# Kernel tuning notes

Measured on AMD Instinct MI355X. Metric: run time of the kernel, lower is better.

Reference implementation:

```python
import jax, jax.numpy as jnp
import numpy as np

WARMUP = 365
# param ranges (lo, hi) standing in for MODEL_PARAM_DICT['tank']['param_range'],
# order: KC W1 W2 K1 K2 a0 b0 c0 h1 h2 a1 a2 h3 b1 h4 c1 d1 e1 e2 h
_RANGES = np.array([
    [0.5, 1.5], [1.0, 100.0], [1.0, 100.0], [0.01, 1.0], [0.01, 1.0],
    [0.01, 1.0], [0.01, 1.0], [0.01, 1.0], [0.0, 90.0], [0.0, 100.0],
    [0.01, 1.0], [0.01, 1.0], [0.0, 100.0], [0.01, 1.0], [0.0, 100.0],
    [0.01, 1.0], [0.001, 1.0], [0.01, 1.0], [0.01, 1.0], [0.0, 100.0],
], dtype=np.float32)


def _tank_sim(p_and_e, parameters):
    lo = jnp.asarray(_RANGES[:, 0])
    hi = jnp.asarray(_RANGES[:, 1])
    ph = lo + parameters * (hi - lo)            # [B, 20] physical params
    (kc, w1, w2, k1, k2, a0, b0, c0p, h1, h2, a1, a2, h3, b1, h4, c1p,
     d1, e1, e2, h) = [ph[:, i] for i in range(20)]

    u = 1.0 / 1000.0        # hydrodt / 1000
    dt = 0.5 * u

    def step(carry, pe_t):
        xf, xp, x2, xs, x3, x4, x5, qs = carry
        p, e = pe_t
        # --- runoff generation (water balance) ---
        ep = kc * e
        et = jnp.minimum(ep, p + xp + xf)
        pe = jnp.clip(p - et, 0.0)
        x = xf
        xf = jnp.clip(x - jnp.clip(ep - p, 0.0), 0.0)
        xp = jnp.clip(xp - jnp.clip(ep - p - x, 0.0), 0.0)
        t1 = jnp.clip(k1 * jnp.minimum(x2, w1 - xp), 0.0)
        xp = xp + t1
        x2 = jnp.clip(x2 - t1, 0.0)
        t2 = jnp.clip(k2 * (xs * w1 - xp * w2) / (w1 + w2), 0.0)
        xp = xp + t2
        xs = jnp.clip(xs - t2, 0.0)
        xf = xf + jnp.clip(xp + pe - w1, 0.0)
        xp = jnp.minimum(w1, xp + pe)
        f1 = a0 * xf
        rs = jnp.where(xf > h2, (xf - h1) * a1 + (xf - h2) * a2,
                       jnp.where(xf > h1, (xf - h1) * a1, 0.0))
        x2 = x2 + f1
        xf = jnp.clip(xf - (rs + f1), 0.0)
        f2 = b0 * x2
        ri = jnp.where(x2 > h3, (x2 - h3) * b1, 0.0)
        x2 = jnp.clip(x2 - (f2 + ri), 0.0)
        x3 = x3 + f2
        f3 = c0p * x3
        rgs = jnp.where(x3 > h4, (x3 - h4) * c1p, 0.0)
        x3 = jnp.clip(x3 - (f3 + rgs), 0.0)
        x4 = x4 + f3
        rgd = d1 * x4
        x4 = jnp.clip(x4 - rgd, 0.0)
        # --- routing ---
        kk0 = jnp.where(x5 >= h, 1.0 / (e1 + e2), 1.0 / e1)
        cc0 = jnp.where(x5 >= h, e2 * h / (e1 + e2), 0.0)
        rk1 = 1.0 / e1
        rc1 = jnp.zeros_like(rk1)
        ii = rs + ri + rgs + rgd
        q1 = jnp.clip((kk0 - dt) / (rk1 + dt) * qs + (ii - rc1 + cc0) / (rk1 + dt), 0.0)
        x5 = rk1 * q1 + rc1
        rk1 = jnp.where(x5 > h, 1.0 / (e1 + e2), rk1)
        rc1 = jnp.where(x5 > h, e2 * h / (e1 + e2), rc1)
        q1 = jnp.clip((kk0 - dt) / (rk1 + dt) * qs + (ii - rc1 + cc0) / (rk1 + dt), 0.0)
        x5 = rk1 * q1 + rc1
        qs = q1
        return (xf, xp, x2, xs, x3, x4, x5, qs), (et, q1)

    prcp = jnp.clip(p_and_e[..., 0], 0.0)   # [T, B]
    pet = jnp.clip(p_and_e[..., 1], 0.0)
    nb = p_and_e.shape[1]
    init = tuple(jnp.full((nb,), 0.01, p_and_e.dtype) for _ in range(8))
    # warmup run (torch.no_grad equivalent: stop_gradient on warm states)
    warm, _ = jax.lax.scan(step, init, (prcp[:WARMUP], pet[:WARMUP]))
    warm = jax.tree_util.tree_map(jax.lax.stop_gradient, warm)
    _, (e_sim, q_sim) = jax.lax.scan(step, warm, (prcp[WARMUP:], pet[WARMUP:]))
    return q_sim[..., None], e_sim[..., None]


def setup_inputs() -> dict:
    key = jax.random.key(0)
    k1, k2 = jax.random.split(key)
    p_and_e = jax.random.uniform(k1, (1096, 16384, 2), dtype=jnp.float32) * 10.0  # mm/d
    parameters = jax.random.uniform(k2, (16384, 20), dtype=jnp.float32)           # normalized [0,1]
    return {"p_and_e": p_and_e, "parameters": parameters}


def reference(p_and_e, parameters):
    return _tank_sim(p_and_e, parameters)
```

## Files before the change

### kernel.cpp

```cpp
#include <hip/hip_runtime.h>
#include <stdint.h>

#define T_TOTAL 1096
#define WARMUP  365
#define NB      16384
#define T_OUT   (T_TOTAL - WARMUP)
#define U       8
#define NG      (T_TOTAL / U)
#define G_STORE 46
#define RS      131072u
#define ORS     65536u
#define EOFF    47906816u

#define KEEP(x) asm volatile("" : "+v"(x))

typedef float f2 __attribute__((ext_vector_type(2)));

#define GLOAD(dst, off) \
    asm volatile("global_load_dwordx2 %0, %1, %2" \
                 : "=v"(dst) : "v"(off), "s"(pe_in))

#define GSTORE(off, val) \
    asm volatile("global_store_dword %0, %1, %2" \
                 :: "v"(off), "v"(val), "s"(out))

#define GROUP(g, CUR, NXT, DO_ET) do {                                        \
        asm volatile("s_waitcnt vmcnt(0)" ::: "memory");                      \
        __builtin_amdgcn_sched_barrier(0);                                    \
        {    \
            const uint32_t t0n = ((g) + 1 < NG) ? (uint32_t)((g) + 1) * (8u * RS) : 0u; \
            _Pragma("unroll")                                                 \
            for (int k = 0; k < U; ++k) {                                     \
                uint32_t o = boff + t0n + (uint32_t)k * RS;                   \
                GLOAD(NXT[k], o);                                             \
            }                                                                 \
        }                                                                     \
        if ((g) >= G_STORE) {                 \
            const int tbP = ((g) - 1) * U - WARMUP;                           \
            _Pragma("unroll")                                                 \
            for (int r = 0; r < U; ++r) {                                     \
                int to = tbP + r; if (to < 0) to = 0;       \
                const uint32_t voq = vb4 + (uint32_t)to * ORS;                \
                const uint32_t voe = voq + EOFF;                              \
                GSTORE(voq, oq[r]);                                           \
                GSTORE(voe, oe[r]);                                           \
            }                                                                 \
        }                                                                     \
        _Pragma("unroll")                                                     \
        for (int r = 0; r < U; ++r) {                                         \
            const float p  = CUR[r].x;      \
            const float e  = CUR[r].y;      \
            const float ep = kc * e;                                          \
            const float pd = p - ep;                                          \
            const float pe = fmaxf(pd, 0.0f);                                 \
            const float d0 = fmaxf(-pd, 0.0f);                                \
            if (DO_ET) oe[r] = fminf(ep, p + (xp + xf));                      \
            const float g0 = fmaxf(d0 - xf, 0.0f);                            \
            xf = fmaxf(xf - d0, 0.0f);                                        \
            xp = fmaxf(xp - g0, 0.0f);                                        \
            const float t1 = k1 * fminf(x2, w1 - xp);                         \
            xp += t1;                                                         \
            x2 = fmaxf(x2 - t1, 0.0f);                                        \
            const float t2 = fmaxf(fmaf(cxs, xs, -(cxp * xp)), 0.0f);         \
            xp += t2;                                                         \
            xs = fmaxf(xs - t2, 0.0f);                                        \
            const float xppe = xp + pe;                                       \
            xf = xf + fmaxf(xppe - w1, 0.0f);                                 \
            xp = fminf(w1, xppe);                                             \
            const float f1v = a0 * xf;                                        \
            const float s1v = fmaf(xf, a1, nh1a1);                            \
            const float s2v = fmaf(xf, a2, nh2a2);                            \
                  \
            const float rsv = fmaxf(s2v, 0.0f) + ((xf > hm) ? s1v : 0.0f);    \
            x2 = x2 + f1v;                                                    \
            xf = fmaxf(xf - (rsv + f1v), 0.0f);                               \
            const float f2v = b0 * x2;                                        \
            const float riv = fmaxf(fmaf(x2, b1, nh3b1), 0.0f);               \
            x2 = fmaxf(x2 - (f2v + riv), 0.0f);                               \
            x3 = x3 + f2v;                                                    \
            const float f3v = c0p * x3;                                       \
            const float rgv = fmaxf(fmaf(x3, c1p, nh4c1), 0.0f);              \
            x3 = fmaxf(x3 - (f3v + rgv), 0.0f);                               \
            x4 = x4 + f3v;                                                    \
            const float rgd = d1 * x4;                                        \
            x4 = fmaxf(x4 - rgd, 0.0f);                                       \
            const bool  c5  = (x5 >= h);                                      \
            const float ii  = (rsv + riv) + (rgv + rgd);                      \
            const float q1B = fmaxf(fmaf(c5 ? gAdB : gBdB, qs,                \
                                         fmaf(ii, dB, c5 ? ccAdB : 0.0f)), 0.0f); \
            const float q1A = fmaxf(fmaf(c5 ? gAdA : gBdA, qs,                \
                                         fmaf(ii, dA, c5 ? 0.0f : nccAdA)), 0.0f); \
            const bool  cb  = (q1B > he1);                                    \
            const float q1  = cb ? q1A : q1B;                                 \
            x5 = cb ? fmaf(kkA, q1A, ccA) : (kkB * q1B);                      \
            qs = q1;                                                          \
            oq[r] = q1;                                                       \
        }                                                                     \
    } while (0)

#define KEEP_CONSTS() do {                                                    \
        KEEP(kc);  KEEP(w1);  KEEP(k1);  KEEP(cxs); KEEP(cxp);                \
        KEEP(a0);  KEEP(b0);  KEEP(c0p); KEEP(hm);                            \
        KEEP(a1);  KEEP(a2);  KEEP(b1);  KEEP(c1p); KEEP(d1);                 \
        KEEP(h);   KEEP(he1);                                                 \
        KEEP(kkA); KEEP(kkB); KEEP(ccA); KEEP(dA);  KEEP(dB);                 \
        KEEP(gAdA); KEEP(gBdA); KEEP(gAdB); KEEP(gBdB);                       \
        KEEP(ccAdB); KEEP(nccAdA);                                            \
        KEEP(nh1a1); KEEP(nh2a2); KEEP(nh3b1); KEEP(nh4c1);                   \
    } while (0)

__global__ __attribute__((amdgpu_flat_work_group_size(64, 64)))
__attribute__((amdgpu_waves_per_eu(1, 1)))
void tank_kernel(
    const float* __restrict__ pe_in,
    const float* __restrict__ params,
    float* __restrict__ out)
{
    const int lane = threadIdx.x;
    const int b    = blockIdx.x * 64 + lane;

    float pn[20];
#pragma unroll
    for (int i = 0; i < 20; ++i) pn[i] = params[b * 20 + i];

    float kc  = 0.5f  + pn[0]  * 1.0f;
    float w1  = 1.0f  + pn[1]  * 99.0f;
    float w2  = 1.0f  + pn[2]  * 99.0f;
    float k1  = 0.01f + pn[3]  * 0.99f;
    float k2  = 0.01f + pn[4]  * 0.99f;
    float a0  = 0.01f + pn[5]  * 0.99f;
    float b0  = 0.01f + pn[6]  * 0.99f;
    float c0p = 0.01f + pn[7]  * 0.99f;
    float h1  = pn[8]  * 90.0f;
    float h2  = pn[9]  * 100.0f;
    float a1  = 0.01f + pn[10] * 0.99f;
    float a2  = 0.01f + pn[11] * 0.99f;
    float h3  = pn[12] * 100.0f;
    float b1  = 0.01f + pn[13] * 0.99f;
    float h4  = pn[14] * 100.0f;
    float c1p = 0.01f + pn[15] * 0.99f;
    float d1  = 0.001f+ pn[16] * 0.999f;
    float e1  = 0.01f + pn[17] * 0.99f;
    float e2  = 0.01f + pn[18] * 0.99f;
    float h   = pn[19] * 100.0f;

    const float dt = 0.5f * (1.0f / 1000.0f);
    float invw = 1.0f / (w1 + w2);
    float cxs  = k2 * w1 * invw;
    float cxp  = k2 * w2 * invw;
    float kkA  = 1.0f / (e1 + e2);
    float kkB  = 1.0f / e1;
    float ccA  = e2 * h * kkA;
    float dA   = 1.0f / (kkA + dt);
    float dB   = 1.0f / (kkB + dt);
    float gAdA = (kkA - dt) * dA, gBdA = (kkB - dt) * dA;
    float gAdB = (kkA - dt) * dB, gBdB = (kkB - dt) * dB;
    float nh1a1 = -h1 * a1;
    float nh2a2 = -h2 * a2;
    float nh3b1 = -h3 * b1;
    float nh4c1 = -h4 * c1p;
    float hm    = fminf(h1, h2);
    float he1   = h * e1;
    float ccAdB = ccA * dB;
    float nccAdA = -ccA * dA;

    float xf = 0.01f, xp = 0.01f, x2 = 0.01f, xs = 0.01f;
    float x3 = 0.01f, x4 = 0.01f, x5 = 0.01f, qs = 0.01f;

    const uint32_t boff = (uint32_t)b * 8u;
    const uint32_t vb4  = (uint32_t)b * 4u;

    f2 bufA[U], bufB[U];
    float oq[U], oe[U];

#pragma unroll
    for (int k = 0; k < U; ++k) {
        uint32_t o = boff + (uint32_t)k * RS;
        GLOAD(bufA[k], o);
    }

#pragma clang loop unroll(disable)
    for (int gp = 0; gp < 22; ++gp) {
        KEEP_CONSTS();
        const int g0i = 2 * gp;
        GROUP(g0i,     bufA, bufB, 0);
        GROUP(g0i + 1, bufB, bufA, 0);
    }
    KEEP_CONSTS();
    GROUP(44, bufA, bufB, 0);
    GROUP(45, bufB, bufA, 1);

#pragma clang loop unroll(disable)
    for (int gp = 0; gp < 46; ++gp) {
        KEEP_CONSTS();
        const int g0i = 46 + 2 * gp;
        GROUP(g0i,     bufA, bufB, 1);
        GROUP(g0i + 1, bufB, bufA, 1);
    }
}

extern "C" void kernel_launch(void* const* d_in, const int* in_sizes, int n_in,
                              void* d_out, int out_size, void* d_ws, size_t ws_size,
                              hipStream_t stream) {
    const float* pe_in  = (const float*)d_in[0];
    const float* params = (const float*)d_in[1];
    float* out = (float*)d_out;

    tank_kernel<<<NB / 64, 64, 0, stream>>>(pe_in, params, out);
}
```

Before: 165.9 us.

## Process two basins per lane with packed f2 math and LDS-staged loads

Each thread now simulates two adjacent basins using two-wide float vectors, so the compiler can emit packed FP32 instructions. The grid is halved to 128 blocks. Input forcing is staged through LDS with global_load_lds in 16-byte chunks instead of per-lane dwordx2 register loads, and outputs are written as dwordx2 stores. This aims to double the arithmetic throughput per instruction on the serial recurrence and widen memory transactions, at the cost of half as many waves to hide latency and higher register pressure.

```diff
diff --git a/kernel.cpp b/kernel.cpp
--- a/kernel.cpp
+++ b/kernel.cpp
@@ -15,84 +15,99 @@
 #define KEEP(x) asm volatile("" : "+v"(x))
 
 typedef float f2 __attribute__((ext_vector_type(2)));
-
-#define GLOAD(dst, off) \
-    asm volatile("global_load_dwordx2 %0, %1, %2" \
-                 : "=v"(dst) : "v"(off), "s"(pe_in))
-
-#define GSTORE(off, val) \
-    asm volatile("global_store_dword %0, %1, %2" \
+typedef float f4 __attribute__((ext_vector_type(4)));
+typedef int   i2 __attribute__((ext_vector_type(2)));
+
+typedef __attribute__((address_space(3))) char      lds_char;
+typedef __attribute__((address_space(3))) uint32_t  lds_u32;
+typedef const __attribute__((address_space(1))) uint32_t glb_u32;
+typedef const __attribute__((address_space(3))) f4       lds_f4;
+
+#define VMAX(a, b) __builtin_elementwise_max(a, b)
+#define VMIN(a, b) __builtin_elementwise_min(a, b)
+#define VFMA(a, b, c) __builtin_elementwise_fma(a, b, c)
+
+#define GSTORE2(off, val) \
+    asm volatile("global_store_dwordx2 %0, %1, %2" \
                  :: "v"(off), "v"(val), "s"(out))
 
-#define GROUP(g, CUR, NXT, DO_ET) do {                                        \
+#define GROUP(g, CUROFF, NXTOFF, DO_ET) do {                                  \
         asm volatile("s_waitcnt vmcnt(0)" ::: "memory");                      \
         __builtin_amdgcn_sched_barrier(0);                                    \
-        {    \
-            const uint32_t t0n = ((g) + 1 < NG) ? (uint32_t)((g) + 1) * (8u * RS) : 0u; \
+        {     \
+            const size_t t0n = ((g) + 1 < NG) ? (size_t)((g) + 1) * (8u * RS) : 0; \
             _Pragma("unroll")                                                 \
-            for (int k = 0; k < U; ++k) {                                     \
-                uint32_t o = boff + t0n + (uint32_t)k * RS;                   \
-                GLOAD(NXT[k], o);                                             \
-            }                                                                 \
+            for (int k = 0; k < U; ++k)                                       \
+                __builtin_amdgcn_global_load_lds(                             \
+                    (glb_u32*)(pe_base + t0n + (size_t)k * RS),               \
+                    (lds_u32*)((lds_char*)smem + (NXTOFF) + k * 1024),        \
+                    16, 0, 0);                                                \
         }                                                                     \
         if ((g) >= G_STORE) {                 \
             const int tbP = ((g) - 1) * U - WARMUP;                           \
             _Pragma("unroll")                                                 \
             for (int r = 0; r < U; ++r) {                                     \
                 int to = tbP + r; if (to < 0) to = 0;       \
-                const uint32_t voq = vb4 + (uint32_t)to * ORS;                \
-                const uint32_t voe = voq + EOFF;                              \
-                GSTORE(voq, oq[r]);                                           \
-                GSTORE(voe, oe[r]);                                           \
+                const uint32_t voq = vb8 + (uint32_t)to * ORS;                \
+                GSTORE2(voq, oq[r]);                                          \
+                GSTORE2(voq + EOFF, oe[r]);                                   \
             }                                                                 \
         }                                                                     \
+        asm volatile("" ::: "memory");                                        \
+             \
+        f4 s[U];                                                              \
+        _Pragma("unroll")                                                     \
+        for (int r = 0; r < U; ++r)                                           \
+            s[r] = *(lds_f4*)((lds_char*)smem + (CUROFF) + r * 1024 + lane16);\
+        _Pragma("unroll")                                                     \
+        for (int r = 0; r < U; ++r) KEEP(s[r]);                               \
         _Pragma("unroll")                                                     \
         for (int r = 0; r < U; ++r) {                                         \
-            const float p  = CUR[r].x;      \
-            const float e  = CUR[r].y;      \
-            const float ep = kc * e;                                          \
-            const float pd = p - ep;                                          \
-            const float pe = fmaxf(pd, 0.0f);                                 \
-            const float d0 = fmaxf(-pd, 0.0f);                                \
-            if (DO_ET) oe[r] = fminf(ep, p + (xp + xf));                      \
-            const float g0 = fmaxf(d0 - xf, 0.0f);                            \
-            xf = fmaxf(xf - d0, 0.0f);                                        \
-            xp = fmaxf(xp - g0, 0.0f);                                        \
-            const float t1 = k1 * fminf(x2, w1 - xp);                         \
+            const f2 p  = s[r].xz;          \
+            const f2 e  = s[r].yw;                                            \
+            const f2 ep = kc * e;                                             \
+            const f2 pd = p - ep;                                             \
+            const f2 pe = VMAX(pd, z2);                                       \
+            const f2 d0 = VMAX(-pd, z2);                                      \
+            if (DO_ET) oe[r] = VMIN(ep, p + (xp + xf));                       \
+            const f2 g0 = VMAX(d0 - xf, z2);                                  \
+            xf = VMAX(xf - d0, z2);                                           \
+            xp = VMAX(xp - g0, z2);                                           \
+            const f2 t1 = k1 * VMIN(x2, w1 - xp);                             \
             xp += t1;                                                         \
-            x2 = fmaxf(x2 - t1, 0.0f);                                        \
-            const float t2 = fmaxf(fmaf(cxs, xs, -(cxp * xp)), 0.0f);         \
+            x2 = VMAX(x2 - t1, z2);                                           \
+            const f2 t2 = VMAX(VFMA(cxs, xs, -(cxp * xp)), z2);               \
             xp += t2;                                                         \
-            xs = fmaxf(xs - t2, 0.0f);                                        \
-            const float xppe = xp + pe;                                       \
-            xf = xf + fmaxf(xppe - w1, 0.0f);                                 \
-            xp = fminf(w1, xppe);                                             \
-            const float f1v = a0 * xf;                                        \
-            const float s1v = fmaf(xf, a1, nh1a1);                            \
-            const float s2v = fmaf(xf, a2, nh2a2);                            \
-                  \
-            const float rsv = fmaxf(s2v, 0.0f) + ((xf > hm) ? s1v : 0.0f);    \
+            xs = VMAX(xs - t2, z2);                                           \
+            const f2 xppe = xp + pe;                                          \
+            xf = xf + VMAX(xppe - w1, z2);                                    \
+            xp = VMIN(w1, xppe);                                              \
+            const f2 f1v = a0 * xf;                                           \
+            const f2 s1v = VFMA(xf, a1, nh1a1);                               \
+            const f2 s2v = VFMA(xf, a2, nh2a2);                               \
+                                          \
+            const f2 rsv = VMAX(s2v, z2) + ((xf > hm) ? s1v : z2);            \
             x2 = x2 + f1v;                                                    \
-            xf = fmaxf(xf - (rsv + f1v), 0.0f);                               \
-            const float f2v = b0 * x2;                                        \
-            const float riv = fmaxf(fmaf(x2, b1, nh3b1), 0.0f);               \
-            x2 = fmaxf(x2 - (f2v + riv), 0.0f);                               \
+            xf = VMAX(xf - (rsv + f1v), z2);                                  \
+            const f2 f2v = b0 * x2;                                           \
+            const f2 riv = VMAX(VFMA(x2, b1, nh3b1), z2);                     \
+            x2 = VMAX(x2 - (f2v + riv), z2);                                  \
             x3 = x3 + f2v;                                                    \
-            const float f3v = c0p * x3;                                       \
-            const float rgv = fmaxf(fmaf(x3, c1p, nh4c1), 0.0f);              \
-            x3 = fmaxf(x3 - (f3v + rgv), 0.0f);                               \
+            const f2 f3v = c0p * x3;                                          \
+            const f2 rgv = VMAX(VFMA(x3, c1p, nh4c1), z2);                    \
+            x3 = VMAX(x3 - (f3v + rgv), z2);                                  \
             x4 = x4 + f3v;                                                    \
-            const float rgd = d1 * x4;                                        \
-            x4 = fmaxf(x4 - rgd, 0.0f);                                       \
-            const bool  c5  = (x5 >= h);                                      \
-            const float ii  = (rsv + riv) + (rgv + rgd);                      \
-            const float q1B = fmaxf(fmaf(c5 ? gAdB : gBdB, qs,                \
-                                         fmaf(ii, dB, c5 ? ccAdB : 0.0f)), 0.0f); \
-            const float q1A = fmaxf(fmaf(c5 ? gAdA : gBdA, qs,                \
-                                         fmaf(ii, dA, c5 ? 0.0f : nccAdA)), 0.0f); \
-            const bool  cb  = (q1B > he1);                                    \
-            const float q1  = cb ? q1A : q1B;                                 \
-            x5 = cb ? fmaf(kkA, q1A, ccA) : (kkB * q1B);                      \
+            const f2 rgd = d1 * x4;                                           \
+            x4 = VMAX(x4 - rgd, z2);                                          \
+            const i2 c5 = x5 >= h;                                            \
+            const f2 ii = (rsv + riv) + (rgv + rgd);                          \
+            const f2 q1B = VMAX(VFMA(c5 ? gAdB : gBdB, qs,                    \
+                                     VFMA(ii, dB, c5 ? ccAdB : z2)), z2);     \
+            const f2 q1A = VMAX(VFMA(c5 ? gAdA : gBdA, qs,                    \
+                                     VFMA(ii, dA, c5 ? z2 : nccAdA)), z2);    \
+            const i2 cb = q1B > he1;                                          \
+            const f2 q1 = cb ? q1A : q1B;                                     \
+            x5 = cb ? VFMA(kkA, q1A, ccA) : (kkB * q1B);                      \
             qs = q1;                                                          \
             oq[r] = q1;                                                       \
         }                                                                     \
@@ -119,83 +134,89 @@
     const int lane = threadIdx.x;
     const int b    = blockIdx.x * 64 + lane;
 
-    float pn[20];
+    __shared__ char smem[16384];
+
+    const float* pp = params + (size_t)(2 * b) * 20;
+    f2 pn[20];
 #pragma unroll
-    for (int i = 0; i < 20; ++i) pn[i] = params[b * 20 + i];
-
-    float kc  = 0.5f  + pn[0]  * 1.0f;
-    float w1  = 1.0f  + pn[1]  * 99.0f;
-    float w2  = 1.0f  + pn[2]  * 99.0f;
-    float k1  = 0.01f + pn[3]  * 0.99f;
-    float k2  = 0.01f + pn[4]  * 0.99f;
-    float a0  = 0.01f + pn[5]  * 0.99f;
-    float b0  = 0.01f + pn[6]  * 0.99f;
-    float c0p = 0.01f + pn[7]  * 0.99f;
-    float h1  = pn[8]  * 90.0f;
-    float h2  = pn[9]  * 100.0f;
-    float a1  = 0.01f + pn[10] * 0.99f;
-    float a2  = 0.01f + pn[11] * 0.99f;
-    float h3  = pn[12] * 100.0f;
-    float b1  = 0.01f + pn[13] * 0.99f;
-    float h4  = pn[14] * 100.0f;
-    float c1p = 0.01f + pn[15] * 0.99f;
-    float d1  = 0.001f+ pn[16] * 0.999f;
-    float e1  = 0.01f + pn[17] * 0.99f;
-    float e2  = 0.01f + pn[18] * 0.99f;
-    float h   = pn[19] * 100.0f;
+    for (int i = 0; i < 20; ++i) pn[i] = (f2){ pp[i], pp[20 + i] };
+
+    const f2 z2 = { 0.0f, 0.0f };
+
+    f2 kc  = 0.5f  + pn[0]  * 1.0f;
+    f2 w1  = 1.0f  + pn[1]  * 99.0f;
+    f2 w2  = 1.0f  + pn[2]  * 99.0f;
+    f2 k1  = 0.01f + pn[3]  * 0.99f;
+    f2 k2  = 0.01f + pn[4]  * 0.99f;
+    f2 a0  = 0.01f + pn[5]  * 0.99f;
+    f2 b0  = 0.01f + pn[6]  * 0.99f;
+    f2 c0p = 0.01f + pn[7]  * 0.99f;
+    f2 h1  = pn[8]  * 90.0f;
+    f2 h2  = pn[9]  * 100.0f;
+    f2 a1  = 0.01f + pn[10] * 0.99f;
+    f2 a2  = 0.01f + pn[11] * 0.99f;
+    f2 h3  = pn[12] * 100.0f;
+    f2 b1  = 0.01f + pn[13] * 0.99f;
+    f2 h4  = pn[14] * 100.0f;
+    f2 c1p = 0.01f + pn[15] * 0.99f;
+    f2 d1  = 0.001f+ pn[16] * 0.999f;
+    f2 e1  = 0.01f + pn[17] * 0.99f;
+    f2 e2  = 0.01f + pn[18] * 0.99f;
+    f2 h   = pn[19] * 100.0f;
 
     const float dt = 0.5f * (1.0f / 1000.0f);
-    float invw = 1.0f / (w1 + w2);
-    float cxs  = k2 * w1 * invw;
-    float cxp  = k2 * w2 * invw;
-    float kkA  = 1.0f / (e1 + e2);
-    float kkB  = 1.0f / e1;
-    float ccA  = e2 * h * kkA;
-    float dA   = 1.0f / (kkA + dt);
-    float dB   = 1.0f / (kkB + dt);
-    float gAdA = (kkA - dt) * dA, gBdA = (kkB - dt) * dA;
-    float gAdB = (kkA - dt) * dB, gBdB = (kkB - dt) * dB;
-    float nh1a1 = -h1 * a1;
-    float nh2a2 = -h2 * a2;
-    float nh3b1 = -h3 * b1;
-    float nh4c1 = -h4 * c1p;
-    float hm    = fminf(h1, h2);
-    float he1   = h * e1;
-    float ccAdB = ccA * dB;
-    float nccAdA = -ccA * dA;
-
-    float xf = 0.01f, xp = 0.01f, x2 = 0.01f, xs = 0.01f;
-    float x3 = 0.01f, x4 = 0.01f, x5 = 0.01f, qs = 0.01f;
-
-    const uint32_t boff = (uint32_t)b * 8u;
-    const uint32_t vb4  = (uint32_t)b * 4u;
-
-    f2 bufA[U], bufB[U];
-    float oq[U], oe[U];
+    f2 invw = 1.0f / (w1 + w2);
+    f2 cxs  = k2 * w1 * invw;
+    f2 cxp  = k2 * w2 * invw;
+    f2 kkA  = 1.0f / (e1 + e2);
+    f2 kkB  = 1.0f / e1;
+    f2 ccA  = e2 * h * kkA;
+    f2 dA   = 1.0f / (kkA + dt);
+    f2 dB   = 1.0f / (kkB + dt);
+    f2 gAdA = (kkA - dt) * dA, gBdA = (kkB - dt) * dA;
+    f2 gAdB = (kkA - dt) * dB, gBdB = (kkB - dt) * dB;
+    f2 nh1a1 = -h1 * a1;
+    f2 nh2a2 = -h2 * a2;
+    f2 nh3b1 = -h3 * b1;
+    f2 nh4c1 = -h4 * c1p;
+    f2 hm    = VMIN(h1, h2);
+    f2 he1   = h * e1;
+    f2 ccAdB = ccA * dB;
+    f2 nccAdA = -ccA * dA;
+
+    f2 xf = {0.01f, 0.01f}, xp = xf, x2 = xf, xs = xf;
+    f2 x3 = xf, x4 = xf, x5 = xf, qs = xf;
+
+    const char* pe_base = (const char*)pe_in + (size_t)blockIdx.x * 1024
+                        + (size_t)lane * 16;
+    const uint32_t lane16 = (uint32_t)lane * 16;
+    const uint32_t vb8    = (uint32_t)b * 8u;
+
+    f2 oq[U], oe[U];
 
 #pragma unroll
-    for (int k = 0; k < U; ++k) {
-        uint32_t o = boff + (uint32_t)k * RS;
-        GLOAD(bufA[k], o);
-    }
+    for (int k = 0; k < U; ++k)
+        __builtin_amdgcn_global_load_lds(
+            (glb_u32*)(pe_base + (size_t)k * RS),
+            (lds_u32*)((lds_char*)smem + k * 1024), 16, 0, 0);
 
 #pragma clang loop unroll(disable)
     for (int gp = 0; gp < 22; ++gp) {
         KEEP_CONSTS();
         const int g0i = 2 * gp;
-        GROUP(g0i,     bufA, bufB, 0);
-        GROUP(g0i + 1, bufB, bufA, 0);
+        GROUP(g0i,     0,    8192, 0);
+        GROUP(g0i + 1, 8192, 0,    0);
     }
     KEEP_CONSTS();
-    GROUP(44, bufA, bufB, 0);
-    GROUP(45, bufB, bufA, 1);
+    GROUP(44, 0,    8192, 0);
+    GROUP(45, 8192, 0,    1);
 
 #pragma clang loop unroll(disable)
     for (int gp = 0; gp < 46; ++gp) {
         KEEP_CONSTS();
         const int g0i = 46 + 2 * gp;
-        GROUP(g0i,     bufA, bufB, 1);
-        GROUP(g0i + 1, bufB, bufA, 1);
+        GROUP(g0i,     0,    8192, 1);
+        GROUP(g0i + 1, 8192, 0,    1);
     }
 }
 
@@ -206,5 +227,5 @@
     const float* params = (const float*)d_in[1];
     float* out = (float*)d_out;
 
-    tank_kernel<<<NB / 64, 64, 0, stream>>>(pe_in, params, out);
+    tank_kernel<<<NB / 128, 64, 0, stream>>>(pe_in, params, out);
 }
```

Result: slower. 236.4 us (+42.5%).
